# Kernel optimization log

Measured on AMD Instinct MI355X. Metric: run time of the kernel, lower is better.

The kernel has to match this reference:

```python
import jax, jax.numpy as jnp
import numpy as np

LN_EPS = 1e-5


def setup_inputs() -> dict:
    key = jax.random.key(0)
    ks = jax.random.split(key, 4)
    S, B, C, V, TS = 512, 64, 1024, 10, 128
    sc = 1.0 / np.sqrt(C)
    return {
        "values": jax.random.normal(ks[0], (S, B, C), dtype=jnp.float32),
        "Wd": jax.random.normal(ks[1], (3, C), dtype=jnp.float32) * sc,
        "bd": jnp.zeros((3,), jnp.float32),
        "Wr": jax.random.normal(ks[2], (2, C), dtype=jnp.float32) * sc,
        "br": jnp.zeros((2,), jnp.float32),
        "ln_g": jnp.ones((C,), jnp.float32),
        "ln_b": jnp.zeros((C,), jnp.float32),
        "Wo": jax.random.normal(ks[3], (V, C), dtype=jnp.float32) * sc,
        "bo": jnp.zeros((V,), jnp.float32),
        "tsize": TS,
    }


def _nam_turing(values, Wd, bd, Wr, br, ln_g, ln_b, Wo, bo, tsize):
    S, B, C = values.shape
    # training-mode addressing: soft softmax over 3 move directions
    directions = jax.nn.softmax(values @ Wd.T + bd, axis=-1)  # [S,B,3]
    rwprobs = jax.nn.sigmoid(values @ Wr.T + br)              # [S,B,2]

    tape0 = jnp.zeros((tsize, B, C), values.dtype)
    pos0 = jnp.zeros((tsize, B), values.dtype).at[0, :].set(1.0)

    def step(carry, xs):
        tape, pos = carry
        v, d, rw = xs  # [B,C], [B,3], [B,2]
        oldval = jnp.einsum("lnc,ln->nc", tape, pos)
        # outer-product write gated by write prob rw[:,1]
        tape = tape + pos[:, :, None] * ((v - oldval) * rw[:, 1:2])[None]
        pos = (jnp.roll(pos, -1, axis=0) * d[None, :, 0]
               + pos * d[None, :, 1]
               + jnp.roll(pos, 1, axis=0) * d[None, :, 2])
        return (tape, pos), None

    (tape, _), _ = jax.lax.scan(step, (tape0, pos0), (values, directions, rwprobs))

    # decoder: LayerNorm -> (dropout as identity) -> Linear
    mu = jnp.mean(tape, axis=-1, keepdims=True)
    var = jnp.mean(jnp.square(tape - mu), axis=-1, keepdims=True)
    h = (tape - mu) * jax.lax.rsqrt(var + LN_EPS) * ln_g + ln_b
    return h @ Wo.T + bo  # [tsize, B, V]


def reference(values, Wd, bd, Wr, br, ln_g, ln_b, Wo, bo, tsize):
    return _nam_turing(values, Wd, bd, Wr, br, ln_g, ln_b, Wo, bo, tsize)
```

## Files before the change

### kernel.cpp

```cpp
#include <hip/hip_runtime.h>
#include <math.h>

#define S_ 512
#define B_ 64
#define C_ 1024
#define T_ 128
#define V_ 10
#define LN_EPS 1e-5f

__global__ __launch_bounds__(256) void k_dirs(const float* __restrict__ values,
                                              const float* __restrict__ Wd,
                                              const float* __restrict__ bd,
                                              const float* __restrict__ Wr,
                                              const float* __restrict__ br,
                                              float* __restrict__ dtr) {
    int wid  = (blockIdx.x << 2) + (threadIdx.x >> 6);
    int lane = threadIdx.x & 63;
    const float4* v4  = (const float4*)(values + (size_t)wid * C_);
    const float4* wd4 = (const float4*)Wd;
    const float4* wr4 = (const float4*)Wr;
    float a0 = 0.f, a1 = 0.f, a2 = 0.f, a3 = 0.f;
#pragma unroll
    for (int k = 0; k < 4; k++) {
        int i = (k << 6) + lane;
        float4 v  = v4[i];
        float4 w0 = wd4[i];
        float4 w1 = wd4[256 + i];
        float4 w2 = wd4[512 + i];
        float4 w3 = wr4[256 + i];
        a0 = fmaf(v.x, w0.x, fmaf(v.y, w0.y, fmaf(v.z, w0.z, fmaf(v.w, w0.w, a0))));
        a1 = fmaf(v.x, w1.x, fmaf(v.y, w1.y, fmaf(v.z, w1.z, fmaf(v.w, w1.w, a1))));
        a2 = fmaf(v.x, w2.x, fmaf(v.y, w2.y, fmaf(v.z, w2.z, fmaf(v.w, w2.w, a2))));
        a3 = fmaf(v.x, w3.x, fmaf(v.y, w3.y, fmaf(v.z, w3.z, fmaf(v.w, w3.w, a3))));
    }
#pragma unroll
    for (int m = 1; m < 64; m <<= 1) {
        a0 += __shfl_xor(a0, m, 64);
        a1 += __shfl_xor(a1, m, 64);
        a2 += __shfl_xor(a2, m, 64);
        a3 += __shfl_xor(a3, m, 64);
    }
    if (lane == 0) {
        float l0 = a0 + bd[0], l1 = a1 + bd[1], l2 = a2 + bd[2];
        float mx = fmaxf(fmaxf(l0, l1), l2);
        float e0 = __expf(l0 - mx), e1 = __expf(l1 - mx), e2 = __expf(l2 - mx);
        float inv = 1.f / (e0 + e1 + e2);
        float r = 1.f / (1.f + __expf(-(a3 + br[1])));
        ((float4*)dtr)[wid] = make_float4(e0 * inv, e1 * inv, e2 * inv, r);
    }
}

__global__ __launch_bounds__(64) void k_pos(const float* __restrict__ dtr,
                                            float* __restrict__ pos_all) {
    int b = blockIdx.x;
    int lane = threadIdx.x;
    const float4* dtr4 = (const float4*)dtr;
    float4 dreg[8];
#pragma unroll
    for (int k = 0; k < 8; k++)
        dreg[k] = dtr4[(((size_t)(k << 6) + lane) << 6) + b];
    float p0 = (lane == 0) ? 1.f : 0.f;
    float p1 = 0.f;
    float* outp = pos_all + ((size_t)b << 7) + lane;
    int up = (lane + 1) & 63, dw = (lane + 63) & 63;
#pragma unroll
    for (int k = 0; k < 8; k++) {
#pragma unroll 4
        for (int tt = 0; tt < 64; tt++) {
            int t = (k << 6) + tt;
            float d0 = __shfl(dreg[k].x, tt, 64);
            float d1 = __shfl(dreg[k].y, tt, 64);
            float d2 = __shfl(dreg[k].z, tt, 64);
            outp[(size_t)t * (B_ * T_)]      = p0;
            outp[(size_t)t * (B_ * T_) + 64] = p1;
            float s0n = __shfl(p0, up, 64), s1n = __shfl(p1, up, 64);
            float s0p = __shfl(p0, dw, 64), s1p = __shfl(p1, dw, 64);
            float up0 = (lane == 63) ? s1n : s0n;
            float dn0 = (lane == 0)  ? s1p : s0p;
            float up1 = (lane == 63) ? s0n : s1n;
            float dn1 = (lane == 0)  ? s0p : s1p;
            p0 = fmaf(up0, d0, fmaf(p0, d1, dn0 * d2));
            p1 = fmaf(up1, d0, fmaf(p1, d1, dn1 * d2));
        }
    }
}

__global__ __launch_bounds__(256, 2) void k_scan(const float* __restrict__ values,
                                                 const float* __restrict__ dtr,
                                                 const float* __restrict__ pos_all,
                                                 float* __restrict__ tape_out) {
    int b    = blockIdx.x >> 3;
    int cblk = blockIdx.x & 7;
    int lane = threadIdx.x & 63;
    int wv   = threadIdx.x >> 6;
    int g    = lane >> 3;
    int cl   = lane & 7;
    int c0   = (cblk << 7) + (wv << 5) + (cl << 2);

    float tape[16][4];
#pragma unroll
    for (int k = 0; k < 16; k++)
#pragma unroll
        for (int j = 0; j < 4; j++) tape[k][j] = 0.f;

    const float4* vp = (const float4*)(values + (size_t)b * C_ + c0);
    const float4* pp = (const float4*)(pos_all + (size_t)b * T_ + (g << 4));
    const int vstride = B_ * C_ / 4;
    const int pstride = B_ * T_ / 4;

    float4 vc = vp[0];
    float4 pc0 = pp[0], pc1 = pp[1], pc2 = pp[2], pc3 = pp[3];
    float rwc = dtr[(size_t)b * 4 + 3];

    for (int t = 0; t < S_; t++) {
        int tn = (t + 1 < S_) ? t + 1 : t;
        size_t vb = (size_t)tn * vstride;
        size_t pb = (size_t)tn * pstride;
        float4 vn  = vp[vb];
        float4 pn0 = pp[pb + 0];
        float4 pn1 = pp[pb + 1];
        float4 pn2 = pp[pb + 2];
        float4 pn3 = pp[pb + 3];
        float rwn = dtr[(((size_t)tn << 6) + b) * 4 + 3];

        float ov0 = 0.f, ov1 = 0.f, ov2 = 0.f, ov3 = 0.f;
        float pk[16];
        pk[0]=pc0.x; pk[1]=pc0.y; pk[2]=pc0.z; pk[3]=pc0.w;
        pk[4]=pc1.x; pk[5]=pc1.y; pk[6]=pc1.z; pk[7]=pc1.w;
        pk[8]=pc2.x; pk[9]=pc2.y; pk[10]=pc2.z; pk[11]=pc2.w;
        pk[12]=pc3.x; pk[13]=pc3.y; pk[14]=pc3.z; pk[15]=pc3.w;
#pragma unroll
        for (int k = 0; k < 16; k++) {
            ov0 = fmaf(tape[k][0], pk[k], ov0);
            ov1 = fmaf(tape[k][1], pk[k], ov1);
            ov2 = fmaf(tape[k][2], pk[k], ov2);
            ov3 = fmaf(tape[k][3], pk[k], ov3);
        }
#pragma unroll
        for (int m = 8; m < 64; m <<= 1) {
            ov0 += __shfl_xor(ov0, m, 64);
            ov1 += __shfl_xor(ov1, m, 64);
            ov2 += __shfl_xor(ov2, m, 64);
            ov3 += __shfl_xor(ov3, m, 64);
        }
        float d0 = (vc.x - ov0) * rwc;
        float d1 = (vc.y - ov1) * rwc;
        float d2 = (vc.z - ov2) * rwc;
        float d3 = (vc.w - ov3) * rwc;
#pragma unroll
        for (int k = 0; k < 16; k++) {
            tape[k][0] = fmaf(pk[k], d0, tape[k][0]);
            tape[k][1] = fmaf(pk[k], d1, tape[k][1]);
            tape[k][2] = fmaf(pk[k], d2, tape[k][2]);
            tape[k][3] = fmaf(pk[k], d3, tape[k][3]);
        }
        vc = vn; rwc = rwn;
        pc0 = pn0; pc1 = pn1; pc2 = pn2; pc3 = pn3;
    }
    float4* tp = (float4*)(tape_out + (size_t)b * C_ + c0);
#pragma unroll
    for (int k = 0; k < 16; k++) {
        int l = (g << 4) + k;
        tp[(size_t)l * vstride] = make_float4(tape[k][0], tape[k][1], tape[k][2], tape[k][3]);
    }
}

__global__ __launch_bounds__(256) void k_out(const float* __restrict__ tape,
                                             const float* __restrict__ ln_g,
                                             const float* __restrict__ ln_b,
                                             const float* __restrict__ Wo,
                                             const float* __restrict__ bo,
                                             float* __restrict__ out) {
    int wid  = (blockIdx.x << 2) + (threadIdx.x >> 6);
    int lane = threadIdx.x & 63;
    const float* tr = tape + (size_t)wid * C_;
    float x[16];
    float s = 0.f, s2 = 0.f;
#pragma unroll
    for (int k = 0; k < 16; k++) {
        x[k] = tr[(k << 6) + lane];
        s += x[k];
        s2 = fmaf(x[k], x[k], s2);
    }
#pragma unroll
    for (int m = 1; m < 64; m <<= 1) {
        s  += __shfl_xor(s,  m, 64);
        s2 += __shfl_xor(s2, m, 64);
    }
    float mu = s * (1.f / C_);
    float var = s2 * (1.f / C_) - mu * mu;
    float rstd = rsqrtf(var + LN_EPS);
    float acc[V_];
#pragma unroll
    for (int v = 0; v < V_; v++) acc[v] = 0.f;
#pragma unroll
    for (int k = 0; k < 16; k++) {
        int cc = (k << 6) + lane;
        float h = fmaf((x[k] - mu) * rstd, ln_g[cc], ln_b[cc]);
#pragma unroll
        for (int v = 0; v < V_; v++) acc[v] = fmaf(h, Wo[v * C_ + cc], acc[v]);
    }
#pragma unroll
    for (int v = 0; v < V_; v++) {
#pragma unroll
        for (int m = 1; m < 64; m <<= 1) acc[v] += __shfl_xor(acc[v], m, 64);
    }
    if (lane == 0) {
#pragma unroll
        for (int v = 0; v < V_; v++) out[(size_t)wid * V_ + v] = acc[v] + bo[v];
    }
}

extern "C" void kernel_launch(void* const* d_in, const int* in_sizes, int n_in,
                              void* d_out, int out_size, void* d_ws, size_t ws_size,
                              hipStream_t stream) {
    const float* values = (const float*)d_in[0];
    const float* Wd     = (const float*)d_in[1];
    const float* bd     = (const float*)d_in[2];
    const float* Wr     = (const float*)d_in[3];
    const float* br     = (const float*)d_in[4];
    const float* ln_g   = (const float*)d_in[5];
    const float* ln_b   = (const float*)d_in[6];
    const float* Wo     = (const float*)d_in[7];
    const float* bo     = (const float*)d_in[8];
    float* out = (float*)d_out;

    float* dtr     = (float*)d_ws;
    float* pos_all = dtr + (size_t)S_ * B_ * 4;
    float* tape    = pos_all + (size_t)S_ * B_ * T_;

    k_dirs<<<dim3((S_ * B_) / 4), dim3(256), 0, stream>>>(values, Wd, bd, Wr, br, dtr);
    k_pos <<<dim3(B_),            dim3(64),  0, stream>>>(dtr, pos_all);
    k_scan<<<dim3(B_ * 8),        dim3(256), 0, stream>>>(values, dtr, pos_all, tape);
    k_out <<<dim3((T_ * B_) / 4), dim3(256), 0, stream>>>(tape, ln_g, ln_b, Wo, bo, out);
}
```

Measured before the change: 597.8 us.

## Block the tape scan over four timesteps using Gram-matrix corrections

The scan kernel now processes four timesteps per iteration. It computes the tape reads for all four steps against the tape as it stood at the start of the block, corrects the later steps with pairwise position dot products (a Gram matrix solved by forward substitution), then applies the four rank-1 updates. This cuts the serial shuffle-reduction chain from one per timestep to one batched reduction per four steps, which shortens the dependency latency. In exchange it adds extra FMAs and shuffles for the Gram terms, raises register pressure, and changes floating-point rounding order.

```diff
diff --git a/kernel.cpp b/kernel.cpp
--- a/kernel.cpp
+++ b/kernel.cpp
@@ -101,67 +101,121 @@
 #pragma unroll
     for (int k = 0; k < 16; k++)
 #pragma unroll
-        for (int j = 0; j < 4; j++) tape[k][j] = 0.f;
+        for (int c = 0; c < 4; c++) tape[k][c] = 0.f;
 
     const float4* vp = (const float4*)(values + (size_t)b * C_ + c0);
     const float4* pp = (const float4*)(pos_all + (size_t)b * T_ + (g << 4));
+    const float*  rp = dtr + (size_t)b * 4 + 3;
     const int vstride = B_ * C_ / 4;
     const int pstride = B_ * T_ / 4;
 
-    float4 vc = vp[0];
-    float4 pc0 = pp[0], pc1 = pp[1], pc2 = pp[2], pc3 = pp[3];
-    float rwc = dtr[(size_t)b * 4 + 3];
-
-    for (int t = 0; t < S_; t++) {
-        int tn = (t + 1 < S_) ? t + 1 : t;
-        size_t vb = (size_t)tn * vstride;
-        size_t pb = (size_t)tn * pstride;
-        float4 vn  = vp[vb];
-        float4 pn0 = pp[pb + 0];
-        float4 pn1 = pp[pb + 1];
-        float4 pn2 = pp[pb + 2];
-        float4 pn3 = pp[pb + 3];
-        float rwn = dtr[(((size_t)tn << 6) + b) * 4 + 3];
-
-        float ov0 = 0.f, ov1 = 0.f, ov2 = 0.f, ov3 = 0.f;
-        float pk[16];
-        pk[0]=pc0.x; pk[1]=pc0.y; pk[2]=pc0.z; pk[3]=pc0.w;
-        pk[4]=pc1.x; pk[5]=pc1.y; pk[6]=pc1.z; pk[7]=pc1.w;
-        pk[8]=pc2.x; pk[9]=pc2.y; pk[10]=pc2.z; pk[11]=pc2.w;
-        pk[12]=pc3.x; pk[13]=pc3.y; pk[14]=pc3.z; pk[15]=pc3.w;
-#pragma unroll
-        for (int k = 0; k < 16; k++) {
-            ov0 = fmaf(tape[k][0], pk[k], ov0);
-            ov1 = fmaf(tape[k][1], pk[k], ov1);
-            ov2 = fmaf(tape[k][2], pk[k], ov2);
-            ov3 = fmaf(tape[k][3], pk[k], ov3);
+    for (int t0 = 0; t0 < S_; t0 += 4) {
+        float4 P[4][4];
+        float4 vv[4];
+        float  rw[4];
+#pragma unroll
+        for (int i = 0; i < 4; i++) {
+#pragma unroll
+            for (int j = 0; j < 4; j++) P[i][j] = pp[i * pstride + j];
+            vv[i] = vp[(size_t)i * vstride];
+            rw[i] = rp[i * (B_ * 4)];
+        }
+        pp += 4 * pstride;
+        vp += (size_t)4 * vstride;
+        rp += 4 * (B_ * 4);
+
+        float a[4][4];
+#pragma unroll
+        for (int i = 0; i < 4; i++)
+#pragma unroll
+            for (int c = 0; c < 4; c++) a[i][c] = 0.f;
+#pragma unroll
+        for (int i = 0; i < 4; i++) {
+#pragma unroll
+            for (int j = 0; j < 4; j++) {
+                float4 q = P[i][j];
+#pragma unroll
+                for (int c = 0; c < 4; c++) {
+                    a[i][c] = fmaf(tape[4 * j + 0][c], q.x, a[i][c]);
+                    a[i][c] = fmaf(tape[4 * j + 1][c], q.y, a[i][c]);
+                    a[i][c] = fmaf(tape[4 * j + 2][c], q.z, a[i][c]);
+                    a[i][c] = fmaf(tape[4 * j + 3][c], q.w, a[i][c]);
+                }
+            }
+        }
+        float G10 = 0.f, G20 = 0.f, G21 = 0.f, G30 = 0.f, G31 = 0.f, G32 = 0.f;
+#pragma unroll
+        for (int j = 0; j < 4; j++) {
+            float4 q0 = P[0][j], q1 = P[1][j], q2 = P[2][j], q3 = P[3][j];
+            G10 = fmaf(q1.x, q0.x, G10); G10 = fmaf(q1.y, q0.y, G10);
+            G10 = fmaf(q1.z, q0.z, G10); G10 = fmaf(q1.w, q0.w, G10);
+            G20 = fmaf(q2.x, q0.x, G20); G20 = fmaf(q2.y, q0.y, G20);
+            G20 = fmaf(q2.z, q0.z, G20); G20 = fmaf(q2.w, q0.w, G20);
+            G21 = fmaf(q2.x, q1.x, G21); G21 = fmaf(q2.y, q1.y, G21);
+            G21 = fmaf(q2.z, q1.z, G21); G21 = fmaf(q2.w, q1.w, G21);
+            G30 = fmaf(q3.x, q0.x, G30); G30 = fmaf(q3.y, q0.y, G30);
+            G30 = fmaf(q3.z, q0.z, G30); G30 = fmaf(q3.w, q0.w, G30);
+            G31 = fmaf(q3.x, q1.x, G31); G31 = fmaf(q3.y, q1.y, G31);
+            G31 = fmaf(q3.z, q1.z, G31); G31 = fmaf(q3.w, q1.w, G31);
+            G32 = fmaf(q3.x, q2.x, G32); G32 = fmaf(q3.y, q2.y, G32);
+            G32 = fmaf(q3.z, q2.z, G32); G32 = fmaf(q3.w, q2.w, G32);
         }
 #pragma unroll
         for (int m = 8; m < 64; m <<= 1) {
-            ov0 += __shfl_xor(ov0, m, 64);
-            ov1 += __shfl_xor(ov1, m, 64);
-            ov2 += __shfl_xor(ov2, m, 64);
-            ov3 += __shfl_xor(ov3, m, 64);
-        }
-        float d0 = (vc.x - ov0) * rwc;
-        float d1 = (vc.y - ov1) * rwc;
-        float d2 = (vc.z - ov2) * rwc;
-        float d3 = (vc.w - ov3) * rwc;
-#pragma unroll
-        for (int k = 0; k < 16; k++) {
-            tape[k][0] = fmaf(pk[k], d0, tape[k][0]);
-            tape[k][1] = fmaf(pk[k], d1, tape[k][1]);
-            tape[k][2] = fmaf(pk[k], d2, tape[k][2]);
-            tape[k][3] = fmaf(pk[k], d3, tape[k][3]);
-        }
-        vc = vn; rwc = rwn;
-        pc0 = pn0; pc1 = pn1; pc2 = pn2; pc3 = pn3;
+#pragma unroll
+            for (int i = 0; i < 4; i++)
+#pragma unroll
+                for (int c = 0; c < 4; c++) a[i][c] += __shfl_xor(a[i][c], m, 64);
+            G10 += __shfl_xor(G10, m, 64);
+            G20 += __shfl_xor(G20, m, 64);
+            G21 += __shfl_xor(G21, m, 64);
+            G30 += __shfl_xor(G30, m, 64);
+            G31 += __shfl_xor(G31, m, 64);
+            G32 += __shfl_xor(G32, m, 64);
+        }
+        float vl[4][4];
+#pragma unroll
+        for (int i = 0; i < 4; i++) {
+            vl[i][0] = vv[i].x; vl[i][1] = vv[i].y; vl[i][2] = vv[i].z; vl[i][3] = vv[i].w;
+        }
+        float del[4][4];
+#pragma unroll
+        for (int c = 0; c < 4; c++) {
+            float d0 = (vl[0][c] - a[0][c]) * rw[0];
+            float s1 = vl[1][c] - a[1][c];
+            s1 = fmaf(-G10, d0, s1);
+            float d1 = s1 * rw[1];
+            float s2 = vl[2][c] - a[2][c];
+            s2 = fmaf(-G20, d0, s2);
+            s2 = fmaf(-G21, d1, s2);
+            float d2 = s2 * rw[2];
+            float s3 = vl[3][c] - a[3][c];
+            s3 = fmaf(-G30, d0, s3);
+            s3 = fmaf(-G31, d1, s3);
+            s3 = fmaf(-G32, d2, s3);
+            float d3 = s3 * rw[3];
+            del[0][c] = d0; del[1][c] = d1; del[2][c] = d2; del[3][c] = d3;
+        }
+#pragma unroll
+        for (int j = 0; j < 4; j++) {
+#pragma unroll
+            for (int i = 0; i < 4; i++) {
+                float4 q = P[i][j];
+#pragma unroll
+                for (int c = 0; c < 4; c++) {
+                    tape[4 * j + 0][c] = fmaf(q.x, del[i][c], tape[4 * j + 0][c]);
+                    tape[4 * j + 1][c] = fmaf(q.y, del[i][c], tape[4 * j + 1][c]);
+                    tape[4 * j + 2][c] = fmaf(q.z, del[i][c], tape[4 * j + 2][c]);
+                    tape[4 * j + 3][c] = fmaf(q.w, del[i][c], tape[4 * j + 3][c]);
+                }
+            }
+        }
     }
     float4* tp = (float4*)(tape_out + (size_t)b * C_ + c0);
 #pragma unroll
     for (int k = 0; k < 16; k++) {
         int l = (g << 4) + k;
-        tp[(size_t)l * vstride] = make_float4(tape[k][0], tape[k][1], tape[k][2], tape[k][3]);
+        tp[(size_t)l * (B_ * C_ / 4)] = make_float4(tape[k][0], tape[k][1], tape[k][2], tape[k][3]);
     }
 }
 
```

After: 608.2 us. No clear change (+1.7%).
